# Optimization experiments

Measured on AMD Instinct MI355X. Metric: run time of the kernel, lower is better.

The kernel has to match this reference:

```python
import jax, jax.numpy as jnp
import numpy as np

B, N, H = 4, 1024, 32


def setup_inputs() -> dict:
    key = jax.random.key(0)
    ks = jax.random.split(key, 8)
    weights = jax.random.uniform(ks[0], (B, N), dtype=jnp.float32)
    distances = jax.random.uniform(ks[1], (B, N, N), dtype=jnp.float32)
    # nn.Linear-style params (kaiming-uniform-ish scale: U(-1/sqrt(fan_in), 1/sqrt(fan_in)))
    def lin(k, fan_in, fan_out):
        k1, k2 = jax.random.split(k)
        bound = 1.0 / np.sqrt(fan_in)
        W = jax.random.uniform(k1, (fan_in, fan_out), minval=-bound, maxval=bound, dtype=jnp.float32)
        b = jax.random.uniform(k2, (fan_out,), minval=-bound, maxval=bound, dtype=jnp.float32)
        return W, b
    W1, b1 = lin(ks[2], 3, H)
    W2, b2 = lin(ks[3], H, H)
    W3, b3 = lin(ks[4], H, 1)
    return {"weights": weights, "distances": distances,
            "W1": W1, "b1": b1, "W2": W2, "b2": b2, "W3": W3, "b3": b3}


def reference(weights, distances, W1, b1, W2, b2, W3, b3):
    # Avoid materializing the stacked [B,N,N,3] tensor: since the first layer
    # is linear, split W1 rows and broadcast-add the three contributions.
    # h1[b,i,j,:] = w_i * W1[0] + w_j * W1[1] + d_ij * W1[2] + b1
    wi = weights[:, :, None, None] * W1[0]            # [B,N,1,H]
    wj = weights[:, None, :, None] * W1[1]            # [B,1,N,H]
    h = wi + wj + distances[..., None] * W1[2] + b1   # [B,N,N,H]
    h = jax.nn.relu(h)
    h = jax.nn.relu(jnp.einsum('bijh,hk->bijk', h, W2) + b2)
    out = jnp.einsum('bijh,ho->bijo', h, W3) + b3     # [B,N,N,1]
    return jax.nn.softplus(out[..., 0])               # [B,N,N]
```

## Files before the change

kernel.cpp:

```cpp
#include <hip/hip_runtime.h>

#define HCH 32
#define NDIM 1024
#define TILE 32
#define SEG 256
#define SEG_ITERS (SEG / TILE)

using half2v   = __attribute__((ext_vector_type(2))) _Float16;
using half8    = __attribute__((ext_vector_type(8))) _Float16;
using floatx16 = __attribute__((ext_vector_type(16))) float;

__global__ __launch_bounds__(256, 4)
void lf_kernel(const float* __restrict__ weights,
               const float* __restrict__ distances,
               const float* __restrict__ W1,
               const float* __restrict__ b1,
               const float* __restrict__ W2,
               const float* __restrict__ b2,
               const float* __restrict__ W3,
               const float* __restrict__ b3,
               float* __restrict__ out)
{
    const int lane = threadIdx.x & 63;
    const int wave_gid = blockIdx.x * 4 + (threadIdx.x >> 6);
    const int row_id = wave_gid >> 2;
    const int seg = wave_gid & 3;
    const int b = row_id >> 10;
    const int j_begin = seg * SEG;

    const int col = lane & 31;
    const int half_id = lane >> 5;
    const int kb = half_id * 8;

    const float wi = weights[row_id];

    half2v base2[8], cc2[8], ee2[8];
#pragma unroll
    for (int p = 0; p < 8; ++p) {
        const int chA = (p < 4) ? (kb + 2 * p) : (16 + kb + 2 * (p - 4));
        const int chB = chA + 1;
        base2[p] = half2v{(_Float16)fmaf(W1[chA], wi, b1[chA]),
                          (_Float16)fmaf(W1[chB], wi, b1[chB])};
        cc2[p] = half2v{(_Float16)W1[HCH + chA], (_Float16)W1[HCH + chB]};
        ee2[p] = half2v{(_Float16)W1[2 * HCH + chA], (_Float16)W1[2 * HCH + chB]};
    }

    half8 a0, a1;
#pragma unroll
    for (int j = 0; j < 8; ++j) {
        a0[j] = (_Float16)W2[(kb + j) * HCH + col];
        a1[j] = (_Float16)W2[(16 + kb + j) * HCH + col];
    }

    floatx16 cinit;
    float w3r[16];
#pragma unroll
    for (int r = 0; r < 16; ++r) {
        const int rc = (r & 3) + 8 * (r >> 2) + 4 * half_id;
        cinit[r] = b2[rc];
        w3r[r]   = W3[rc];
    }
    const float b3v = b3[0];

    const float* __restrict__ drow = distances + (size_t)row_id * NDIM;
    const float* __restrict__ wrow = weights + b * NDIM;
    float* __restrict__ orow = out + (size_t)row_id * NDIM;

    float d_t[SEG_ITERS], wj_t[SEG_ITERS];
#pragma unroll
    for (int t = 0; t < SEG_ITERS; ++t) {
        d_t[t]  = drow[j_begin + t * TILE + col];
        wj_t[t] = wrow[j_begin + t * TILE + col];
    }

    const half2v zero2 = half2v{(_Float16)0.0f, (_Float16)0.0f};

#pragma unroll
    for (int t = 0; t < SEG_ITERS; ++t) {
        const int j0 = j_begin + t * TILE;

        const _Float16 dh  = (_Float16)d_t[t];
        const _Float16 wjh = (_Float16)wj_t[t];
        const half2v d2  = half2v{dh, dh};
        const half2v wj2 = half2v{wjh, wjh};

        union Frag { half8 v; half2v h[4]; } u0, u1;
#pragma unroll
        for (int p = 0; p < 4; ++p) {
            half2v t0 = __builtin_elementwise_fma(cc2[p], wj2, base2[p]);
            t0 = __builtin_elementwise_fma(ee2[p], d2, t0);
            u0.h[p] = __builtin_elementwise_max(t0, zero2);
            half2v t1 = __builtin_elementwise_fma(cc2[p + 4], wj2, base2[p + 4]);
            t1 = __builtin_elementwise_fma(ee2[p + 4], d2, t1);
            u1.h[p] = __builtin_elementwise_max(t1, zero2);
        }

        floatx16 acc = __builtin_amdgcn_mfma_f32_32x32x16_f16(a0, u0.v, cinit, 0, 0, 0);
        acc = __builtin_amdgcn_mfma_f32_32x32x16_f16(a1, u1.v, acc, 0, 0, 0);

        float s0 = 0.0f, s1 = 0.0f, s2 = 0.0f, s3 = 0.0f;
#pragma unroll
        for (int r = 0; r < 16; r += 4) {
            s0 = fmaf(fmaxf(acc[r + 0], 0.0f), w3r[r + 0], s0);
            s1 = fmaf(fmaxf(acc[r + 1], 0.0f), w3r[r + 1], s1);
            s2 = fmaf(fmaxf(acc[r + 2], 0.0f), w3r[r + 2], s2);
            s3 = fmaf(fmaxf(acc[r + 3], 0.0f), w3r[r + 3], s3);
        }
        float s = (s0 + s1) + (s2 + s3);
        s += __shfl_xor(s, 32, 64);

        const float x = s + b3v;
        const float sp = fmaxf(x, 0.0f) + __logf(1.0f + __expf(-fabsf(x)));

        if (lane < 32) orow[j0 + col] = sp;
    }
}

extern "C" void kernel_launch(void* const* d_in, const int* in_sizes, int n_in,
                              void* d_out, int out_size, void* d_ws, size_t ws_size,
                              hipStream_t stream) {
    const float* weights   = (const float*)d_in[0];
    const float* distances = (const float*)d_in[1];
    const float* W1 = (const float*)d_in[2];
    const float* b1 = (const float*)d_in[3];
    const float* W2 = (const float*)d_in[4];
    const float* b2 = (const float*)d_in[5];
    const float* W3 = (const float*)d_in[6];
    const float* b3 = (const float*)d_in[7];
    float* out = (float*)d_out;

    const int rows_total = 4 * 1024;
    dim3 grid(rows_total * (NDIM / SEG) / 4);
    lf_kernel<<<grid, 256, 0, stream>>>(weights, distances, W1, b1, W2, b2, W3, b3, out);
}
```

Before: 107.5 us.

## Switch to 16x16x32 MFMA tiles with doubled segment and prefetched distance loads

Replaces the 32x32x16 MFMA with four 16x16x32 MFMAs per 32-column step, so each lane needs only one K-slice of the first-layer activations and fewer half2 FMAs per column. Each wave now covers 512 columns instead of 256, which halves the grid and the per-wave setup cost per output. The loads of all distance and weight values before the loop are replaced by a two-stage rolling prefetch. The final reduction needs extra cross-lane shuffles, the wrap-around prefetch issues a few redundant loads, and the longer segment means fewer waves to hide memory latency.

```diff
diff --git a/kernel.cpp b/kernel.cpp
--- a/kernel.cpp
+++ b/kernel.cpp
@@ -2,13 +2,12 @@
 
 #define HCH 32
 #define NDIM 1024
-#define TILE 32
-#define SEG 256
-#define SEG_ITERS (SEG / TILE)
+#define SEG 512
+#define ITERS (SEG / 32)
 
-using half2v   = __attribute__((ext_vector_type(2))) _Float16;
-using half8    = __attribute__((ext_vector_type(8))) _Float16;
-using floatx16 = __attribute__((ext_vector_type(16))) float;
+using half2v  = __attribute__((ext_vector_type(2))) _Float16;
+using half8   = __attribute__((ext_vector_type(8))) _Float16;
+using floatx4 = __attribute__((ext_vector_type(4))) float;
 
 __global__ __launch_bounds__(256, 4)
 void lf_kernel(const float* __restrict__ weights,
@@ -22,22 +21,21 @@
                float* __restrict__ out)
 {
     const int lane = threadIdx.x & 63;
-    const int wave_gid = blockIdx.x * 4 + (threadIdx.x >> 6);
-    const int row_id = wave_gid >> 2;
-    const int seg = wave_gid & 3;
+    const int wave_gid = __builtin_amdgcn_readfirstlane(blockIdx.x * 4 + (threadIdx.x >> 6));
+    const int row_id = wave_gid >> 1;
+    const int j_begin = (wave_gid & 1) * SEG;
     const int b = row_id >> 10;
-    const int j_begin = seg * SEG;
 
-    const int col = lane & 31;
-    const int half_id = lane >> 5;
-    const int kb = half_id * 8;
+    const int px = lane & 15;
+    const int quad = lane >> 4;
+    const int kb = quad * 8;
 
     const float wi = weights[row_id];
 
-    half2v base2[8], cc2[8], ee2[8];
+    half2v base2[4], cc2[4], ee2[4];
 #pragma unroll
-    for (int p = 0; p < 8; ++p) {
-        const int chA = (p < 4) ? (kb + 2 * p) : (16 + kb + 2 * (p - 4));
+    for (int p = 0; p < 4; ++p) {
+        const int chA = kb + 2 * p;
         const int chB = chA + 1;
         base2[p] = half2v{(_Float16)fmaf(W1[chA], wi, b1[chA]),
                           (_Float16)fmaf(W1[chB], wi, b1[chB])};
@@ -45,74 +43,90 @@
         ee2[p] = half2v{(_Float16)W1[2 * HCH + chA], (_Float16)W1[2 * HCH + chB]};
     }
 
-    half8 a0, a1;
+    half8 a_lo, a_hi;
 #pragma unroll
     for (int j = 0; j < 8; ++j) {
-        a0[j] = (_Float16)W2[(kb + j) * HCH + col];
-        a1[j] = (_Float16)W2[(16 + kb + j) * HCH + col];
+        a_lo[j] = (_Float16)W2[(kb + j) * HCH + px];
+        a_hi[j] = (_Float16)W2[(kb + j) * HCH + 16 + px];
     }
 
-    floatx16 cinit;
-    float w3r[16];
+    floatx4 ci_lo, ci_hi;
+    float w3lo[4], w3hi[4];
 #pragma unroll
-    for (int r = 0; r < 16; ++r) {
-        const int rc = (r & 3) + 8 * (r >> 2) + 4 * half_id;
-        cinit[r] = b2[rc];
-        w3r[r]   = W3[rc];
+    for (int r = 0; r < 4; ++r) {
+        ci_lo[r] = b2[quad * 4 + r];
+        ci_hi[r] = b2[16 + quad * 4 + r];
+        w3lo[r]  = W3[quad * 4 + r];
+        w3hi[r]  = W3[16 + quad * 4 + r];
     }
     const float b3v = b3[0];
 
-    const float* __restrict__ drow = distances + (size_t)row_id * NDIM;
-    const float* __restrict__ wrow = weights + b * NDIM;
-    float* __restrict__ orow = out + (size_t)row_id * NDIM;
+    const float* __restrict__ drow = distances + (size_t)row_id * NDIM + j_begin;
+    const float* __restrict__ wrow = weights + b * NDIM + j_begin;
+    float* __restrict__ orow = out + (size_t)row_id * NDIM + j_begin;
 
-    float d_t[SEG_ITERS], wj_t[SEG_ITERS];
+    float dbuf[2][2], wbuf[2][2];
 #pragma unroll
-    for (int t = 0; t < SEG_ITERS; ++t) {
-        d_t[t]  = drow[j_begin + t * TILE + col];
-        wj_t[t] = wrow[j_begin + t * TILE + col];
+    for (int t = 0; t < 2; ++t) {
+        dbuf[t][0] = drow[t * 32 + px];
+        dbuf[t][1] = drow[t * 32 + 16 + px];
+        wbuf[t][0] = wrow[t * 32 + px];
+        wbuf[t][1] = wrow[t * 32 + 16 + px];
     }
 
     const half2v zero2 = half2v{(_Float16)0.0f, (_Float16)0.0f};
 
 #pragma unroll
-    for (int t = 0; t < SEG_ITERS; ++t) {
-        const int j0 = j_begin + t * TILE;
+    for (int t = 0; t < ITERS; ++t) {
+        const int cur = t & 1;
+        const float dA = dbuf[cur][0], dB = dbuf[cur][1];
+        const float wA = wbuf[cur][0], wB = wbuf[cur][1];
 
-        const _Float16 dh  = (_Float16)d_t[t];
-        const _Float16 wjh = (_Float16)wj_t[t];
-        const half2v d2  = half2v{dh, dh};
-        const half2v wj2 = half2v{wjh, wjh};
+        const int tp = (t + 2 < ITERS) ? (t + 2) : (t + 2 - ITERS);
+        dbuf[cur][0] = drow[tp * 32 + px];
+        dbuf[cur][1] = drow[tp * 32 + 16 + px];
+        wbuf[cur][0] = wrow[tp * 32 + px];
+        wbuf[cur][1] = wrow[tp * 32 + 16 + px];
 
-        union Frag { half8 v; half2v h[4]; } u0, u1;
+        const _Float16 dhA = (_Float16)dA, whA = (_Float16)wA;
+        const _Float16 dhB = (_Float16)dB, whB = (_Float16)wB;
+        const half2v d2A = half2v{dhA, dhA}, w2A = half2v{whA, whA};
+        const half2v d2B = half2v{dhB, dhB}, w2B = half2v{whB, whB};
+
+        union Frag { half8 v; half2v h[4]; } fA, fB;
 #pragma unroll
         for (int p = 0; p < 4; ++p) {
-            half2v t0 = __builtin_elementwise_fma(cc2[p], wj2, base2[p]);
-            t0 = __builtin_elementwise_fma(ee2[p], d2, t0);
-            u0.h[p] = __builtin_elementwise_max(t0, zero2);
-            half2v t1 = __builtin_elementwise_fma(cc2[p + 4], wj2, base2[p + 4]);
-            t1 = __builtin_elementwise_fma(ee2[p + 4], d2, t1);
-            u1.h[p] = __builtin_elementwise_max(t1, zero2);
+            half2v tA = __builtin_elementwise_fma(cc2[p], w2A, base2[p]);
+            tA = __builtin_elementwise_fma(ee2[p], d2A, tA);
+            fA.h[p] = __builtin_elementwise_max(tA, zero2);
+            half2v tB = __builtin_elementwise_fma(cc2[p], w2B, base2[p]);
+            tB = __builtin_elementwise_fma(ee2[p], d2B, tB);
+            fB.h[p] = __builtin_elementwise_max(tB, zero2);
         }
 
-        floatx16 acc = __builtin_amdgcn_mfma_f32_32x32x16_f16(a0, u0.v, cinit, 0, 0, 0);
-        acc = __builtin_amdgcn_mfma_f32_32x32x16_f16(a1, u1.v, acc, 0, 0, 0);
+        floatx4 aAlo = __builtin_amdgcn_mfma_f32_16x16x32_f16(a_lo, fA.v, ci_lo, 0, 0, 0);
+        floatx4 aAhi = __builtin_amdgcn_mfma_f32_16x16x32_f16(a_hi, fA.v, ci_hi, 0, 0, 0);
+        floatx4 aBlo = __builtin_amdgcn_mfma_f32_16x16x32_f16(a_lo, fB.v, ci_lo, 0, 0, 0);
+        floatx4 aBhi = __builtin_amdgcn_mfma_f32_16x16x32_f16(a_hi, fB.v, ci_hi, 0, 0, 0);
 
-        float s0 = 0.0f, s1 = 0.0f, s2 = 0.0f, s3 = 0.0f;
+        float sA = 0.0f, sB = 0.0f;
 #pragma unroll
-        for (int r = 0; r < 16; r += 4) {
-            s0 = fmaf(fmaxf(acc[r + 0], 0.0f), w3r[r + 0], s0);
-            s1 = fmaf(fmaxf(acc[r + 1], 0.0f), w3r[r + 1], s1);
-            s2 = fmaf(fmaxf(acc[r + 2], 0.0f), w3r[r + 2], s2);
-            s3 = fmaf(fmaxf(acc[r + 3], 0.0f), w3r[r + 3], s3);
+        for (int r = 0; r < 4; ++r) {
+            sA = fmaf(fmaxf(aAlo[r], 0.0f), w3lo[r], sA);
+            sA = fmaf(fmaxf(aAhi[r], 0.0f), w3hi[r], sA);
+            sB = fmaf(fmaxf(aBlo[r], 0.0f), w3lo[r], sB);
+            sB = fmaf(fmaxf(aBhi[r], 0.0f), w3hi[r], sB);
         }
-        float s = (s0 + s1) + (s2 + s3);
-        s += __shfl_xor(s, 32, 64);
+        sA += __shfl_xor(sA, 16, 64);
+        sA += __shfl_xor(sA, 32, 64);
+        sB += __shfl_xor(sB, 16, 64);
+        sB += __shfl_xor(sB, 32, 64);
 
-        const float x = s + b3v;
+        const float s_sel = (lane & 16) ? sB : sA;
+        const float x = s_sel + b3v;
         const float sp = fmaxf(x, 0.0f) + __logf(1.0f + __expf(-fabsf(x)));
 
-        if (lane < 32) orow[j0 + col] = sp;
+        if (lane < 32) orow[t * 32 + lane] = sp;
     }
 }
 
```

Result: faster. 105.3 us (-2.1%).
